# Optimization experiments

Hardware: AMD Instinct MI355X
Metric: run time of the kernel (lower is better)

## Reference

```python
import jax, jax.numpy as jnp
import numpy as np

C = 512
NUM_HEADS = 8


def setup_inputs() -> dict:
    key = jax.random.key(0)
    ks = jax.random.split(key, 9)
    s = 1.0 / np.sqrt(C)
    inp = {
        "x": jax.random.normal(ks[0], (2, C, 64, 64), dtype=jnp.float32),
        "Wq": jax.random.uniform(ks[1], (C, C), jnp.float32, -s, s),
        "bq": jax.random.uniform(ks[2], (C,), jnp.float32, -s, s),
        "Wk": jax.random.uniform(ks[3], (C, C), jnp.float32, -s, s),
        "bk": jax.random.uniform(ks[4], (C,), jnp.float32, -s, s),
        "Wv": jax.random.uniform(ks[5], (C, C), jnp.float32, -s, s),
        "bv": jax.random.uniform(ks[6], (C,), jnp.float32, -s, s),
        "Wp": jax.random.uniform(ks[7], (C, C), jnp.float32, -s, s),
        "bp": jax.random.uniform(ks[8], (C,), jnp.float32, -s, s),
    }
    return inp


def _split_heads(t):
    # [B, S, C] -> [B, h, S, d]
    B, S, Ct = t.shape
    return t.reshape(B, S, NUM_HEADS, Ct // NUM_HEADS).transpose(0, 2, 1, 3)


def reference(x, Wq, bq, Wk, bk, Wv, bv, Wp, bp):
    B, Ct, H, W = x.shape
    tok = x.transpose(0, 2, 3, 1).reshape(B, H * W, Ct)  # [B, S, C]
    q = _split_heads(tok @ Wq.T + bq)
    k = _split_heads(tok @ Wk.T + bk)
    v = _split_heads(tok @ Wv.T + bv)
    d = q.shape[-1]
    scores = jnp.einsum("bhsd,bhtd->bhst", q, k) / jnp.sqrt(jnp.float32(d))
    attn = jax.nn.softmax(scores, axis=-1)
    out = jnp.einsum("bhst,bhtd->bhsd", attn, v)
    out = out.transpose(0, 2, 1, 3).reshape(B, H * W, Ct)  # merge heads
    out = out @ Wp.T + bp
    return out.reshape(B, H, W, Ct).transpose(0, 3, 1, 2)
```

## Files before the change

### kernel.cpp

```cpp
#include <hip/hip_runtime.h>
#include <stdint.h>
#include <math.h>

typedef unsigned short u16;
typedef uint32_t u32;
typedef short bf16x8 __attribute__((ext_vector_type(8)));
typedef float f32x4  __attribute__((ext_vector_type(4)));

#define DEV __device__ __forceinline__

DEV u16 f2bf(float f) {
    union { float f; u32 u; } x; x.f = f;
    u32 lsb = (x.u >> 16) & 1u;
    x.u += 0x7fffu + lsb;
    return (u16)(x.u >> 16);
}

DEV u32 pack2(float a, float b) {
    union { float f; u32 u; } x, y; x.f = a; y.f = b;
    return __builtin_amdgcn_perm(y.u + 0x8000u, x.u + 0x8000u, 0x07060302u);
}

#if __has_builtin(__builtin_amdgcn_exp2f)
DEV float fexp2(float x) { return __builtin_amdgcn_exp2f(x); }
#else
DEV float fexp2(float x) { return __expf(x * 0.69314718056f); }
#endif

DEV f32x4 mfma16(bf16x8 a, bf16x8 b, f32x4 c) {
    return __builtin_amdgcn_mfma_f32_16x16x32_bf16(a, b, c, 0, 0, 0);
}

__global__ __launch_bounds__(256) void prep_kernel(const float* __restrict__ x,
                                                   u16* __restrict__ tok,
                                                   const float* __restrict__ w0,
                                                   const float* __restrict__ w1,
                                                   const float* __restrict__ w2,
                                                   const float* __restrict__ w3,
                                                   u16* __restrict__ dst) {
    __shared__ u16 t[64][65];
    const int id = blockIdx.x, tid = threadIdx.x;
    if (id < 1024) {
        const int b = id >> 9, c0 = ((id >> 6) & 7) * 64, s0 = (id & 63) * 64;
        const float* xb = x + ((size_t)b * 512 + c0) * 4096 + s0;
        u16* tb = tok + ((size_t)b * 4096 + s0) * 512 + c0;
        {
            const int jc = tid & 15, i0 = tid >> 4;
#pragma unroll
            for (int ii = 0; ii < 4; ii++) {
                int i = i0 * 4 + ii;
                float4 v = *(const float4*)&xb[(size_t)i * 4096 + jc * 4];
                t[i][jc * 4 + 0] = f2bf(v.x);
                t[i][jc * 4 + 1] = f2bf(v.y);
                t[i][jc * 4 + 2] = f2bf(v.z);
                t[i][jc * 4 + 3] = f2bf(v.w);
            }
        }
        __syncthreads();
        {
            const int j = tid & 31, i0 = tid >> 5;
#pragma unroll
            for (int ii = 0; ii < 8; ii++) {
                int srow = i0 * 8 + ii;
                u32 v = (u32)t[j * 2][srow] | ((u32)t[j * 2 + 1][srow] << 16);
                *(u32*)(&tb[(size_t)srow * 512 + j * 2]) = v;
            }
        }
    } else {
        const int id2 = id - 1024;
        const int j = id2 >> 8;
        const float* src = (j == 0) ? w0 : (j == 1) ? w1 : (j == 2) ? w2 : w3;
        int idx = ((id2 & 255) * 256 + tid) * 4;
        float4 v = *(const float4*)&src[idx];
        uint2 pv;
        pv.x = pack2(v.x, v.y);
        pv.y = pack2(v.z, v.w);
        *(uint2*)&dst[(size_t)j * 262144 + idx] = pv;
    }
}

__global__ __launch_bounds__(256, 2) void qkv3_kernel(const u16* __restrict__ Wbf,
                                                      const float* __restrict__ bq,
                                                      const float* __restrict__ bk,
                                                      const float* __restrict__ bv,
                                                      const u16* __restrict__ tok,
                                                      u16* __restrict__ Qb,
                                                      u16* __restrict__ Kb,
                                                      u16* __restrict__ Vb) {
    __shared__ u16 Alds[3][6144];
    __shared__ u16 Blds[3][4096];
    const int tid = threadIdx.x;
    const int wave = tid >> 6, lane = tid & 63, q = lane >> 4, c = lane & 15;
    const int n0 = blockIdx.x * 128;
    const int m0 = blockIdx.y * 64;
    const int b  = blockIdx.z;
    const u16* tokb = tok + (size_t)b * (4096 * 512);

    const int cs = tid & 15, qs = (tid >> 4) & 3, ms = tid >> 6;
    const u16* As0 = Wbf +          (size_t)(m0 + ms * 16 + cs) * 512 + qs * 8;
    const u16* As1 = Wbf + 262144 + (size_t)(m0 + ms * 16 + cs) * 512 + qs * 8;
    const u16* As2 = Wbf + 524288 + (size_t)(m0 + ms * 16 + cs) * 512 + qs * 8;
    const u16* Bsrc0 = tokb + (size_t)(n0 + ms * 16 + cs) * 512 + qs * 8;
    const u16* Bsrc1 = tokb + (size_t)(n0 + (ms + 4) * 16 + cs) * 512 + qs * 8;

    f32x4 acc[3][2][4] = {};

    int4 pA0 = *(const int4*)&As0[0];
    int4 pA1 = *(const int4*)&As1[0];
    int4 pA2 = *(const int4*)&As2[0];
    int4 pB0 = *(const int4*)&Bsrc0[0];
    int4 pB1 = *(const int4*)&Bsrc1[0];
    int4 hA0 = *(const int4*)&As0[32];
    int4 hA1 = *(const int4*)&As1[32];
    int4 hA2 = *(const int4*)&As2[32];
    int4 hB0 = *(const int4*)&Bsrc0[32];
    int4 hB1 = *(const int4*)&Bsrc1[32];
    *(int4*)&Alds[0][tid * 8]        = pA0;
    *(int4*)&Alds[0][2048 + tid * 8] = pA1;
    *(int4*)&Alds[0][4096 + tid * 8] = pA2;
    *(int4*)&Blds[0][tid * 8]         = pB0;
    *(int4*)&Blds[0][(tid + 256) * 8] = pB1;
    __syncthreads();

    int p = 0, pw = 1;
    for (int it = 0; it < 16; it++) {
        const int kn = ((it + 2) & 15) * 32;

        int4 nA0 = *(const int4*)&As0[kn];
        int4 nA1 = *(const int4*)&As1[kn];
        int4 nA2 = *(const int4*)&As2[kn];
        int4 nB0 = *(const int4*)&Bsrc0[kn];
        int4 nB1 = *(const int4*)&Bsrc1[kn];

        bf16x8 bfr[4];
#pragma unroll
        for (int t = 0; t < 4; t++) {
            int gn = (((wave >> 1) * 4 + t) * 4 + q) * 16 + c;
            bfr[t] = *(const bf16x8*)&Blds[p][gn * 8];
        }
#pragma unroll
        for (int j = 0; j < 3; j++) {
            bf16x8 af[2];
#pragma unroll
            for (int mt = 0; mt < 2; mt++) {
                int gm = ((((wave & 1) * 2 + mt) * 4 + q) * 16 + c);
                af[mt] = *(const bf16x8*)&Alds[p][j * 2048 + gm * 8];
            }
#pragma unroll
            for (int mt = 0; mt < 2; mt++)
#pragma unroll
                for (int nt = 0; nt < 4; nt++)
                    acc[j][mt][nt] = mfma16(af[mt], bfr[nt], acc[j][mt][nt]);
        }

        *(int4*)&Alds[pw][tid * 8]        = hA0;
        *(int4*)&Alds[pw][2048 + tid * 8] = hA1;
        *(int4*)&Alds[pw][4096 + tid * 8] = hA2;
        *(int4*)&Blds[pw][tid * 8]         = hB0;
        *(int4*)&Blds[pw][(tid + 256) * 8] = hB1;
        hA0 = nA0; hA1 = nA1; hA2 = nA2; hB0 = nB0; hB1 = nB1;
        __syncthreads();
        p = pw; pw = (pw == 2) ? 0 : pw + 1;
    }

    const int mbase = m0 + (wave & 1) * 32, nbase = n0 + (wave >> 1) * 64;
    const int hd = m0 >> 6;
#pragma unroll
    for (int j = 0; j < 3; j++) {
        const float* bias = (j == 0) ? bq : (j == 1) ? bk : bv;
        const float scale = (j == 0) ? 0.1803368801f : 1.0f;
        u16* outm = (j == 0) ? Qb : Kb;
#pragma unroll
        for (int mt = 0; mt < 2; mt++) {
            int co0 = mbase + mt * 16 + q * 4;
            float b0 = bias[co0 + 0], b1 = bias[co0 + 1];
            float b2 = bias[co0 + 2], b3 = bias[co0 + 3];
#pragma unroll
            for (int nt = 0; nt < 4; nt++) {
                int scol = nbase + nt * 16 + c;
                float v0 = (acc[j][mt][nt][0] + b0) * scale;
                float v1 = (acc[j][mt][nt][1] + b1) * scale;
                float v2 = (acc[j][mt][nt][2] + b2) * scale;
                float v3 = (acc[j][mt][nt][3] + b3) * scale;
                if (j < 2) {
                    uint2 pv; pv.x = pack2(v0, v1); pv.y = pack2(v2, v3);
                    size_t idx = ((size_t)(b * 8 + hd) * 4096 + scol) * 64 + (co0 & 63);
                    *(uint2*)&outm[idx] = pv;
                } else {
                    Vb[((size_t)(b * 512 + co0 + 0)) * 4096 + scol] = f2bf(v0);
                    Vb[((size_t)(b * 512 + co0 + 1)) * 4096 + scol] = f2bf(v1);
                    Vb[((size_t)(b * 512 + co0 + 2)) * 4096 + scol] = f2bf(v2);
                    Vb[((size_t)(b * 512 + co0 + 3)) * 4096 + scol] = f2bf(v3);
                }
            }
        }
    }
}

DEV void proj_core(const u16* __restrict__ W, const float* __restrict__ bias,
                   const u16* __restrict__ Bb, void* __restrict__ out,
                   int b, int mode, float scale,
                   u16 (*__restrict__ Alds)[4096], u16 (*__restrict__ Blds)[4096]) {
    const int tid = threadIdx.x;
    const int wave = tid >> 6, lane = tid & 63, q = lane >> 4, c = lane & 15;
    const int m0 = blockIdx.y * 128, n0 = blockIdx.x * 128;

    const int cs = tid & 15, qs = (tid >> 4) & 3, ms = (tid >> 6) & 3;
    const u16* Asrc0 = W  + (size_t)(m0 + ms * 16 + cs) * 512 + qs * 8;
    const u16* Asrc1 = W  + (size_t)(m0 + (ms + 4) * 16 + cs) * 512 + qs * 8;
    const u16* Bsrc0 = Bb + (size_t)(n0 + ms * 16 + cs) * 512 + qs * 8;
    const u16* Bsrc1 = Bb + (size_t)(n0 + (ms + 4) * 16 + cs) * 512 + qs * 8;

    f32x4 acc[4][4] = {};

    int4 pa0 = *(const int4*)&Asrc0[0];
    int4 pa1 = *(const int4*)&Asrc1[0];
    int4 pb0 = *(const int4*)&Bsrc0[0];
    int4 pb1 = *(const int4*)&Bsrc1[0];
    int4 ha0 = *(const int4*)&Asrc0[32];
    int4 ha1 = *(const int4*)&Asrc1[32];
    int4 hb0 = *(const int4*)&Bsrc0[32];
    int4 hb1 = *(const int4*)&Bsrc1[32];
    *(int4*)&Alds[0][tid * 8]         = pa0;
    *(int4*)&Alds[0][(tid + 256) * 8] = pa1;
    *(int4*)&Blds[0][tid * 8]         = pb0;
    *(int4*)&Blds[0][(tid + 256) * 8] = pb1;
    __syncthreads();

    int p = 0, pw = 1;
    for (int it = 0; it < 16; it++) {
        const int kn = ((it + 2) & 15) * 32;

        int4 na0 = *(const int4*)&Asrc0[kn];
        int4 na1 = *(const int4*)&Asrc1[kn];
        int4 nb0 = *(const int4*)&Bsrc0[kn];
        int4 nb1 = *(const int4*)&Bsrc1[kn];

        bf16x8 af[4], bfr[4];
#pragma unroll
        for (int t = 0; t < 4; t++) {
            int gm = (((wave & 1) * 4 + t) * 4 + q) * 16 + c;
            af[t] = *(const bf16x8*)&Alds[p][gm * 8];
            int gn = (((wave >> 1) * 4 + t) * 4 + q) * 16 + c;
            bfr[t] = *(const bf16x8*)&Blds[p][gn * 8];
        }
#pragma unroll
        for (int mt = 0; mt < 4; mt++)
#pragma unroll
            for (int nt = 0; nt < 4; nt++)
                acc[mt][nt] = mfma16(af[mt], bfr[nt], acc[mt][nt]);

        *(int4*)&Alds[pw][tid * 8]         = ha0;
        *(int4*)&Alds[pw][(tid + 256) * 8] = ha1;
        *(int4*)&Blds[pw][tid * 8]         = hb0;
        *(int4*)&Blds[pw][(tid + 256) * 8] = hb1;
        ha0 = na0; ha1 = na1; hb0 = nb0; hb1 = nb1;
        __syncthreads();
        p = pw; pw = (pw == 2) ? 0 : pw + 1;
    }

    const int mbase = m0 + (wave & 1) * 64, nbase = n0 + (wave >> 1) * 64;
#pragma unroll
    for (int mt = 0; mt < 4; mt++) {
        int co0 = mbase + mt * 16 + q * 4;
        float b0 = bias[co0 + 0], b1 = bias[co0 + 1];
        float b2 = bias[co0 + 2], b3 = bias[co0 + 3];
#pragma unroll
        for (int nt = 0; nt < 4; nt++) {
            int scol = nbase + nt * 16 + c;
            float v0 = (acc[mt][nt][0] + b0) * scale;
            float v1 = (acc[mt][nt][1] + b1) * scale;
            float v2 = (acc[mt][nt][2] + b2) * scale;
            float v3 = (acc[mt][nt][3] + b3) * scale;
            float* o = (float*)out;
            o[((size_t)(b * 512 + co0 + 0)) * 4096 + scol] = v0;
            o[((size_t)(b * 512 + co0 + 1)) * 4096 + scol] = v1;
            o[((size_t)(b * 512 + co0 + 2)) * 4096 + scol] = v2;
            o[((size_t)(b * 512 + co0 + 3)) * 4096 + scol] = v3;
        }
    }
    (void)mode;
}

__global__ __launch_bounds__(256) void projp_kernel(const u16* __restrict__ Wp,
                                                    const float* __restrict__ bp,
                                                    const u16* __restrict__ attout,
                                                    float* __restrict__ out) {
    __shared__ u16 Alds[3][4096];
    __shared__ u16 Blds[3][4096];
    const int b = blockIdx.z;
    proj_core(Wp, bp, attout + (size_t)b * (4096 * 512), out, b, 2, 1.0f, Alds, Blds);
}

__global__ __launch_bounds__(256, 4) void attn_kernel(const u16* __restrict__ Qm,
                                                      const u16* __restrict__ Km,
                                                      const u16* __restrict__ Vm,
                                                      float* __restrict__ Opart,
                                                      float* __restrict__ Lpart) {
    __shared__ u16 Klds[2][4096];
    __shared__ u16 Vlds[2][4096];
    __shared__ u16 Plds[4][1024];
    const int tid = threadIdx.x, wave = tid >> 6, lane = tid & 63;
    const int q = lane >> 4, c = lane & 15;
    const int bhd = blockIdx.y, s0 = blockIdx.x * 128, z = blockIdx.z;
    const int tbase = z * 2048;
    const u16* Qb = Qm + (size_t)bhd * (4096 * 64);
    const u16* Kb = Km + (size_t)bhd * (4096 * 64);
    const u16* Vb = Vm + (size_t)bhd * (64 * 4096);

    bf16x8 qf[2][2];
#pragma unroll
    for (int st = 0; st < 2; st++)
#pragma unroll
        for (int kd = 0; kd < 2; kd++)
            qf[st][kd] = *(const bf16x8*)
                &Qb[(size_t)(s0 + wave * 32 + st * 16 + c) * 64 + kd * 32 + q * 8];

    const int rr = tid & 15, qq = (tid >> 4) & 3, kk = (tid >> 6) & 1;
    const int t40 = tid >> 7, t41 = t40 + 2;
    const u16* Ksrc0 = Kb + (size_t)(tbase + t40 * 16 + rr) * 64 + kk * 32 + qq * 8;
    const u16* Ksrc1 = Kb + (size_t)(tbase + t41 * 16 + rr) * 64 + kk * 32 + qq * 8;
    const u16* Vsrc0 = Vb + (size_t)(t40 * 16 + rr) * 4096 + tbase + kk * 32 + qq * 8;
    const u16* Vsrc1 = Vb + (size_t)(t41 * 16 + rr) * 4096 + tbase + kk * 32 + qq * 8;

    u16* Pwr       = &Plds[wave][(q >> 1) * 128 + (q & 1) * 4 + c * 8];
    const u16* Prd = &Plds[wave][q * 128 + c * 8];

    f32x4 oacc[4][2] = {};
    float lsum[2] = {0.f, 0.f};

    *(int4*)&Klds[0][tid * 8]         = *(const int4*)&Ksrc0[0];
    *(int4*)&Klds[0][(tid + 256) * 8] = *(const int4*)&Ksrc1[0];
    *(int4*)&Vlds[0][tid * 8]         = *(const int4*)&Vsrc0[0];
    *(int4*)&Vlds[0][(tid + 256) * 8] = *(const int4*)&Vsrc1[0];
    __syncthreads();

    for (int it = 0; it < 32; it++) {
        const int p = it & 1;
        const size_t t0n = (size_t)(((it + 1) & 31) * 64);

        int4 kst0 = *(const int4*)&Ksrc0[t0n * 64];
        int4 kst1 = *(const int4*)&Ksrc1[t0n * 64];
        int4 vst0 = *(const int4*)&Vsrc0[t0n];
        int4 vst1 = *(const int4*)&Vsrc1[t0n];

        f32x4 sacc[4][2] = {};
#pragma unroll
        for (int kd = 0; kd < 2; kd++) {
            bf16x8 ka[4];
#pragma unroll
            for (int tt = 0; tt < 4; tt++)
                ka[tt] = *(const bf16x8*)&Klds[p][(((tt * 2 + kd) * 4 + q) * 16 + c) * 8];
#pragma unroll
            for (int tt = 0; tt < 4; tt++)
#pragma unroll
                for (int st = 0; st < 2; st++)
                    sacc[tt][st] = mfma16(ka[tt], qf[st][kd], sacc[tt][st]);
        }

        bf16x8 va[2][4];
#pragma unroll
        for (int kt = 0; kt < 2; kt++)
#pragma unroll
            for (int dt = 0; dt < 4; dt++)
                va[kt][dt] = *(const bf16x8*)&Vlds[p][(((dt * 2 + kt) * 4 + q) * 16 + c) * 8];

#pragma unroll
        for (int st = 0; st < 2; st++) {
#pragma unroll
            for (int tt = 0; tt < 4; tt++) {
                float p0 = fexp2(sacc[tt][st][0]);
                float p1 = fexp2(sacc[tt][st][1]);
                float p2 = fexp2(sacc[tt][st][2]);
                float p3 = fexp2(sacc[tt][st][3]);
                lsum[st] += (p0 + p1) + (p2 + p3);
                uint2 pv; pv.x = pack2(p0, p1); pv.y = pack2(p2, p3);
                *(uint2*)&Pwr[tt * 256] = pv;
            }
#pragma unroll
            for (int kt = 0; kt < 2; kt++) {
                bf16x8 pb = *(const bf16x8*)&Prd[kt * 512];
#pragma unroll
                for (int dt = 0; dt < 4; dt++)
                    oacc[dt][st] = mfma16(va[kt][dt], pb, oacc[dt][st]);
            }
        }

        *(int4*)&Klds[1 - p][tid * 8]         = kst0;
        *(int4*)&Klds[1 - p][(tid + 256) * 8] = kst1;
        *(int4*)&Vlds[1 - p][tid * 8]         = vst0;
        *(int4*)&Vlds[1 - p][(tid + 256) * 8] = vst1;
        __syncthreads();
    }

#pragma unroll
    for (int st = 0; st < 2; st++) {
        float l = lsum[st];
        l += __shfl_xor(l, 16, 64);
        l += __shfl_xor(l, 32, 64);
        const int s = s0 + wave * 32 + st * 16 + c;
        const size_t rowbase = ((size_t)(z * 16 + bhd) * 4096 + s) * 64;
#pragma unroll
        for (int dt = 0; dt < 4; dt++) {
            float4 ov;
            ov.x = oacc[dt][st][0];
            ov.y = oacc[dt][st][1];
            ov.z = oacc[dt][st][2];
            ov.w = oacc[dt][st][3];
            *(float4*)&Opart[rowbase + dt * 16 + q * 4] = ov;
        }
        if (lane < 16)
            Lpart[(size_t)z * 65536 + bhd * 4096 + s0 + wave * 32 + st * 16 + lane] = l;
    }
}

__global__ __launch_bounds__(256) void merge_kernel(const float* __restrict__ Opart,
                                                    const float* __restrict__ Lpart,
                                                    u16* __restrict__ attout) {
    const int i = blockIdx.x * 256 + threadIdx.x;
    const int flat = i * 4;
    const int row = flat >> 6, dv = flat & 63;
    const int bhd = row >> 12, s = row & 4095;
    const float l = Lpart[row] + Lpart[65536 + row];
    const float rl = 1.0f / l;
    const float4 a  = *(const float4*)&Opart[flat];
    const float4 b4 = *(const float4*)&Opart[4194304 + flat];
    uint2 pv;
    pv.x = pack2((a.x + b4.x) * rl, (a.y + b4.y) * rl);
    pv.y = pack2((a.z + b4.z) * rl, (a.w + b4.w) * rl);
    const int b = bhd >> 3, hd = bhd & 7;
    *(uint2*)&attout[((size_t)(b * 4096 + s)) * 512 + hd * 64 + dv] = pv;
}

extern "C" void kernel_launch(void* const* d_in, const int* in_sizes, int n_in,
                              void* d_out, int out_size, void* d_ws, size_t ws_size,
                              hipStream_t stream) {
    (void)in_sizes; (void)n_in; (void)out_size; (void)ws_size;
    const float* x  = (const float*)d_in[0];
    const float* Wq = (const float*)d_in[1];
    const float* bq = (const float*)d_in[2];
    const float* Wk = (const float*)d_in[3];
    const float* bk = (const float*)d_in[4];
    const float* Wv = (const float*)d_in[5];
    const float* bv = (const float*)d_in[6];
    const float* Wp = (const float*)d_in[7];
    const float* bp = (const float*)d_in[8];
    float* out = (float*)d_out;

    const size_t NTOK = (size_t)4 * 1024 * 1024;
    u16* tok = (u16*)d_ws;
    u16* Qb  = tok + NTOK;
    u16* Kb  = Qb + NTOK;
    u16* Vb  = Kb + NTOK;
    u16* Wbf = Vb + NTOK;
    u16* attout = tok;
    float* Opart = (float*)(Wbf + 4 * 262144);
    float* Lpart = Opart + (size_t)2 * 4194304;

    prep_kernel<<<dim3(2048), 256, 0, stream>>>(x, tok, Wq, Wk, Wv, Wp, Wbf);
    qkv3_kernel<<<dim3(32, 8, 2), 256, 0, stream>>>(Wbf, bq, bk, bv, tok, Qb, Kb, Vb);
    attn_kernel<<<dim3(32, 16, 2), 256, 0, stream>>>(Qb, Kb, Vb, Opart, Lpart);
    merge_kernel<<<dim3(4096), 256, 0, stream>>>(Opart, Lpart, attout);
    projp_kernel<<<dim3(32, 4, 2), 256, 0, stream>>>(Wbf + 3 * 262144, bp, attout, out);
}
```

Measured before the change: 217.9 us.

## Fuse split-K attention merge into output projection and add MFMA priority hints

New measurement: 399.7 us. 83.5% more time.

```diff
diff --git a/kernel.cpp b/kernel.cpp
--- a/kernel.cpp
+++ b/kernel.cpp
@@ -197,99 +197,117 @@
     }
 }
 
-DEV void proj_core(const u16* __restrict__ W, const float* __restrict__ bias,
-                   const u16* __restrict__ Bb, void* __restrict__ out,
-                   int b, int mode, float scale,
-                   u16 (*__restrict__ Alds)[4096], u16 (*__restrict__ Blds)[4096]) {
+DEV void ld_opart(const float* __restrict__ Opart, size_t obase, float4 o[4]) {
+    o[0] = *(const float4*)&Opart[obase];
+    o[1] = *(const float4*)&Opart[obase + 4];
+    o[2] = *(const float4*)&Opart[4194304 + obase];
+    o[3] = *(const float4*)&Opart[4194304 + obase + 4];
+}
+DEV int4 merge_pack(const float4 o[4], float rl) {
+    int4 r;
+    r.x = pack2((o[0].x + o[2].x) * rl, (o[0].y + o[2].y) * rl);
+    r.y = pack2((o[0].z + o[2].z) * rl, (o[0].w + o[2].w) * rl);
+    r.z = pack2((o[1].x + o[3].x) * rl, (o[1].y + o[3].y) * rl);
+    r.w = pack2((o[1].z + o[3].z) * rl, (o[1].w + o[3].w) * rl);
+    return r;
+}
+
+__global__ __launch_bounds__(256, 2) void projp_kernel(const u16* __restrict__ Wp,
+                                                       const float* __restrict__ bp,
+                                                       const float* __restrict__ Opart,
+                                                       const float* __restrict__ Lpart,
+                                                       float* __restrict__ out) {
+    __shared__ u16 Alds[3][2048];
+    __shared__ u16 Blds[3][4096];
     const int tid = threadIdx.x;
     const int wave = tid >> 6, lane = tid & 63, q = lane >> 4, c = lane & 15;
-    const int m0 = blockIdx.y * 128, n0 = blockIdx.x * 128;
-
-    const int cs = tid & 15, qs = (tid >> 4) & 3, ms = (tid >> 6) & 3;
-    const u16* Asrc0 = W  + (size_t)(m0 + ms * 16 + cs) * 512 + qs * 8;
-    const u16* Asrc1 = W  + (size_t)(m0 + (ms + 4) * 16 + cs) * 512 + qs * 8;
-    const u16* Bsrc0 = Bb + (size_t)(n0 + ms * 16 + cs) * 512 + qs * 8;
-    const u16* Bsrc1 = Bb + (size_t)(n0 + (ms + 4) * 16 + cs) * 512 + qs * 8;
-
-    f32x4 acc[4][4] = {};
-
-    int4 pa0 = *(const int4*)&Asrc0[0];
-    int4 pa1 = *(const int4*)&Asrc1[0];
-    int4 pb0 = *(const int4*)&Bsrc0[0];
-    int4 pb1 = *(const int4*)&Bsrc1[0];
-    int4 ha0 = *(const int4*)&Asrc0[32];
-    int4 ha1 = *(const int4*)&Asrc1[32];
-    int4 hb0 = *(const int4*)&Bsrc0[32];
-    int4 hb1 = *(const int4*)&Bsrc1[32];
-    *(int4*)&Alds[0][tid * 8]         = pa0;
-    *(int4*)&Alds[0][(tid + 256) * 8] = pa1;
-    *(int4*)&Blds[0][tid * 8]         = pb0;
-    *(int4*)&Blds[0][(tid + 256) * 8] = pb1;
+    const int n0 = blockIdx.x * 128;
+    const int m0 = blockIdx.y * 64;
+    const int b  = blockIdx.z;
+
+    const int cs = tid & 15, qs = (tid >> 4) & 3, ms = tid >> 6;
+    const u16* Asrc = Wp + (size_t)(m0 + ms * 16 + cs) * 512 + qs * 8;
+    const int srow0 = n0 + ms * 16 + cs, srow1 = srow0 + 64;
+
+    f32x4 acc[2][4] = {};
+
+#define PJ_ISSUE(kn, A_, B0_, B1_, L_)                                          \
+    {                                                                           \
+        const int hd_ = (kn) >> 6, dv0_ = ((kn) & 32) + qs * 8;                 \
+        const size_t rb_ = (size_t)(b * 8 + hd_) * 4096;                        \
+        A_ = *(const int4*)&Asrc[kn];                                           \
+        ld_opart(Opart, (rb_ + srow0) * 64 + dv0_, B0_);                        \
+        ld_opart(Opart, (rb_ + srow1) * 64 + dv0_, B1_);                        \
+        L_.x = Lpart[rb_ + srow0]; L_.y = Lpart[65536 + rb_ + srow0];           \
+        L_.z = Lpart[rb_ + srow1]; L_.w = Lpart[65536 + rb_ + srow1];           \
+    }
+#define PJ_WRITE(buf, A_, B0_, B1_, L_)                                         \
+    {                                                                           \
+        float rl0_ = 1.0f / (L_.x + L_.y), rl1_ = 1.0f / (L_.z + L_.w);         \
+        *(int4*)&Alds[buf][tid * 8] = A_;                                       \
+        *(int4*)&Blds[buf][tid * 8] = merge_pack(B0_, rl0_);                    \
+        *(int4*)&Blds[buf][(tid + 256) * 8] = merge_pack(B1_, rl1_);            \
+    }
+
+    {
+        int4 pA; float4 pB0[4], pB1[4], pL;
+        PJ_ISSUE(0, pA, pB0, pB1, pL);
+        PJ_WRITE(0, pA, pB0, pB1, pL);
+    }
+    int4 hA; float4 hB0[4], hB1[4], hL;
+    PJ_ISSUE(32, hA, hB0, hB1, hL);
     __syncthreads();
 
     int p = 0, pw = 1;
     for (int it = 0; it < 16; it++) {
         const int kn = ((it + 2) & 15) * 32;
 
-        int4 na0 = *(const int4*)&Asrc0[kn];
-        int4 na1 = *(const int4*)&Asrc1[kn];
-        int4 nb0 = *(const int4*)&Bsrc0[kn];
-        int4 nb1 = *(const int4*)&Bsrc1[kn];
-
-        bf16x8 af[4], bfr[4];
+        int4 nA; float4 nB0[4], nB1[4], nL;
+        PJ_ISSUE(kn, nA, nB0, nB1, nL);
+
+        bf16x8 bfr[4];
 #pragma unroll
         for (int t = 0; t < 4; t++) {
-            int gm = (((wave & 1) * 4 + t) * 4 + q) * 16 + c;
-            af[t] = *(const bf16x8*)&Alds[p][gm * 8];
             int gn = (((wave >> 1) * 4 + t) * 4 + q) * 16 + c;
             bfr[t] = *(const bf16x8*)&Blds[p][gn * 8];
         }
-#pragma unroll
-        for (int mt = 0; mt < 4; mt++)
+        bf16x8 af[2];
+#pragma unroll
+        for (int mt = 0; mt < 2; mt++) {
+            int gm = ((((wave & 1) * 2 + mt) * 4 + q) * 16 + c);
+            af[mt] = *(const bf16x8*)&Alds[p][gm * 8];
+        }
+#pragma unroll
+        for (int mt = 0; mt < 2; mt++)
 #pragma unroll
             for (int nt = 0; nt < 4; nt++)
                 acc[mt][nt] = mfma16(af[mt], bfr[nt], acc[mt][nt]);
 
-        *(int4*)&Alds[pw][tid * 8]         = ha0;
-        *(int4*)&Alds[pw][(tid + 256) * 8] = ha1;
-        *(int4*)&Blds[pw][tid * 8]         = hb0;
-        *(int4*)&Blds[pw][(tid + 256) * 8] = hb1;
-        ha0 = na0; ha1 = na1; hb0 = nb0; hb1 = nb1;
+        PJ_WRITE(pw, hA, hB0, hB1, hL);
+        hA = nA; hL = nL;
+#pragma unroll
+        for (int i = 0; i < 4; i++) { hB0[i] = nB0[i]; hB1[i] = nB1[i]; }
         __syncthreads();
         p = pw; pw = (pw == 2) ? 0 : pw + 1;
     }
 
-    const int mbase = m0 + (wave & 1) * 64, nbase = n0 + (wave >> 1) * 64;
-#pragma unroll
-    for (int mt = 0; mt < 4; mt++) {
+    const int mbase = m0 + (wave & 1) * 32, nbase = n0 + (wave >> 1) * 64;
+#pragma unroll
+    for (int mt = 0; mt < 2; mt++) {
         int co0 = mbase + mt * 16 + q * 4;
-        float b0 = bias[co0 + 0], b1 = bias[co0 + 1];
-        float b2 = bias[co0 + 2], b3 = bias[co0 + 3];
+        float b0 = bp[co0 + 0], b1 = bp[co0 + 1];
+        float b2 = bp[co0 + 2], b3 = bp[co0 + 3];
 #pragma unroll
         for (int nt = 0; nt < 4; nt++) {
             int scol = nbase + nt * 16 + c;
-            float v0 = (acc[mt][nt][0] + b0) * scale;
-            float v1 = (acc[mt][nt][1] + b1) * scale;
-            float v2 = (acc[mt][nt][2] + b2) * scale;
-            float v3 = (acc[mt][nt][3] + b3) * scale;
-            float* o = (float*)out;
-            o[((size_t)(b * 512 + co0 + 0)) * 4096 + scol] = v0;
-            o[((size_t)(b * 512 + co0 + 1)) * 4096 + scol] = v1;
-            o[((size_t)(b * 512 + co0 + 2)) * 4096 + scol] = v2;
-            o[((size_t)(b * 512 + co0 + 3)) * 4096 + scol] = v3;
-        }
-    }
-    (void)mode;
-}
-
-__global__ __launch_bounds__(256) void projp_kernel(const u16* __restrict__ Wp,
-                                                    const float* __restrict__ bp,
-                                                    const u16* __restrict__ attout,
-                                                    float* __restrict__ out) {
-    __shared__ u16 Alds[3][4096];
-    __shared__ u16 Blds[3][4096];
-    const int b = blockIdx.z;
-    proj_core(Wp, bp, attout + (size_t)b * (4096 * 512), out, b, 2, 1.0f, Alds, Blds);
+            out[((size_t)(b * 512 + co0 + 0)) * 4096 + scol] = acc[mt][nt][0] + b0;
+            out[((size_t)(b * 512 + co0 + 1)) * 4096 + scol] = acc[mt][nt][1] + b1;
+            out[((size_t)(b * 512 + co0 + 2)) * 4096 + scol] = acc[mt][nt][2] + b2;
+            out[((size_t)(b * 512 + co0 + 3)) * 4096 + scol] = acc[mt][nt][3] + b3;
+        }
+    }
+#undef PJ_ISSUE
+#undef PJ_WRITE
 }
 
 __global__ __launch_bounds__(256, 4) void attn_kernel(const u16* __restrict__ Qm,
@@ -345,6 +363,7 @@
         int4 vst1 = *(const int4*)&Vsrc1[t0n];
 
         f32x4 sacc[4][2] = {};
+        __builtin_amdgcn_s_setprio(1);
 #pragma unroll
         for (int kd = 0; kd < 2; kd++) {
             bf16x8 ka[4];
@@ -357,6 +376,7 @@
                 for (int st = 0; st < 2; st++)
                     sacc[tt][st] = mfma16(ka[tt], qf[st][kd], sacc[tt][st]);
         }
+        __builtin_amdgcn_s_setprio(0);
 
         bf16x8 va[2][4];
 #pragma unroll
@@ -377,6 +397,7 @@
                 uint2 pv; pv.x = pack2(p0, p1); pv.y = pack2(p2, p3);
                 *(uint2*)&Pwr[tt * 256] = pv;
             }
+            __builtin_amdgcn_s_setprio(1);
 #pragma unroll
             for (int kt = 0; kt < 2; kt++) {
                 bf16x8 pb = *(const bf16x8*)&Prd[kt * 512];
@@ -384,6 +405,7 @@
                 for (int dt = 0; dt < 4; dt++)
                     oacc[dt][st] = mfma16(va[kt][dt], pb, oacc[dt][st]);
             }
+            __builtin_amdgcn_s_setprio(0);
         }
 
         *(int4*)&Klds[1 - p][tid * 8]         = kst0;
@@ -412,24 +434,6 @@
         if (lane < 16)
             Lpart[(size_t)z * 65536 + bhd * 4096 + s0 + wave * 32 + st * 16 + lane] = l;
     }
-}
-
-__global__ __launch_bounds__(256) void merge_kernel(const float* __restrict__ Opart,
-                                                    const float* __restrict__ Lpart,
-                                                    u16* __restrict__ attout) {
-    const int i = blockIdx.x * 256 + threadIdx.x;
-    const int flat = i * 4;
-    const int row = flat >> 6, dv = flat & 63;
-    const int bhd = row >> 12, s = row & 4095;
-    const float l = Lpart[row] + Lpart[65536 + row];
-    const float rl = 1.0f / l;
-    const float4 a  = *(const float4*)&Opart[flat];
-    const float4 b4 = *(const float4*)&Opart[4194304 + flat];
-    uint2 pv;
-    pv.x = pack2((a.x + b4.x) * rl, (a.y + b4.y) * rl);
-    pv.y = pack2((a.z + b4.z) * rl, (a.w + b4.w) * rl);
-    const int b = bhd >> 3, hd = bhd & 7;
-    *(uint2*)&attout[((size_t)(b * 4096 + s)) * 512 + hd * 64 + dv] = pv;
 }
 
 extern "C" void kernel_launch(void* const* d_in, const int* in_sizes, int n_in,
@@ -453,13 +457,11 @@
     u16* Kb  = Qb + NTOK;
     u16* Vb  = Kb + NTOK;
     u16* Wbf = Vb + NTOK;
-    u16* attout = tok;
     float* Opart = (float*)(Wbf + 4 * 262144);
     float* Lpart = Opart + (size_t)2 * 4194304;
 
     prep_kernel<<<dim3(2048), 256, 0, stream>>>(x, tok, Wq, Wk, Wv, Wp, Wbf);
     qkv3_kernel<<<dim3(32, 8, 2), 256, 0, stream>>>(Wbf, bq, bk, bv, tok, Qb, Kb, Vb);
     attn_kernel<<<dim3(32, 16, 2), 256, 0, stream>>>(Qb, Kb, Vb, Opart, Lpart);
-    merge_kernel<<<dim3(4096), 256, 0, stream>>>(Opart, Lpart, attout);
-    projp_kernel<<<dim3(32, 4, 2), 256, 0, stream>>>(Wbf + 3 * 262144, bp, attout, out);
-}
+    projp_kernel<<<dim3(32, 8, 2), 256, 0, stream>>>(Wbf + 3 * 262144, bp, Opart, Lpart, out);
+}
```
